# Optimization experiments

Hardware: AMD Instinct MI355X
Metric: run time of the kernel (lower is better)

The kernel has to match this reference:

```python
import jax, jax.numpy as jnp
import numpy as np

B, S, D, H, L, V, NP, GH = 2, 1024, 1024, 16, 6, 32000, 16, 64
DH = D // H
FF = int(D * 4 * 2 / 3)  # SwiGLU hidden = int(dim*ffn_expansion*2/3)


def setup_inputs() -> dict:
    key = jax.random.key(0)
    ks = jax.random.split(key, 12)
    n = lambda k, shp, s=0.02: (jax.random.normal(k, shp, jnp.float32) * s)
    # per-layer memory gate init: -3.0 .. -1.0 across layers
    gate_init = jnp.array([-3.0 + (i / (L - 1)) * 2.0 for i in range(L)], jnp.float32)
    return dict(
        input_ids=jax.random.randint(ks[0], (B, S), 0, V),
        tok_emb=n(ks[1], (V, D)),
        w_init=jnp.zeros((D,), jnp.float32),
        persistent=n(ks[2], (NP, D), 1.0),
        norm1_w=jnp.ones((L, D), jnp.float32),
        norm2_w=jnp.ones((L, D), jnp.float32),
        norm_f_w=jnp.ones((D,), jnp.float32),
        qkv_w=n(ks[3], (L, 3 * D, D)),
        q_norm_w=jnp.ones((L, DH), jnp.float32),
        k_norm_w=jnp.ones((L, DH), jnp.float32),
        gamma_w1=n(ks[4], (L, GH, D)),
        gamma_w2=n(ks[5], (L, 1, GH)),
        memory_gate=gate_init,
        w_o=n(ks[6], (L, D, D), 0.02 / 2 ** 0.5),
        ffn_w1=n(ks[7], (L, FF, D)),
        ffn_w2=n(ks[8], (L, FF, D)),
        ffn_w3=n(ks[9], (L, D, FF)),
    )


def _rms(x, w, eps=1e-6):
    return x * jax.lax.rsqrt(jnp.mean(x * x, axis=-1, keepdims=True) + eps) * w


def _rope_tables():
    inv_freq = 1.0 / (10000.0 ** (jnp.arange(0, DH, 2, dtype=jnp.float32) / DH))
    t = jnp.arange(S, dtype=jnp.float32)
    freqs = jnp.einsum('s,f->sf', t, inv_freq)  # (S, DH/2)
    return jnp.cos(freqs), jnp.sin(freqs)


def _rope(x, cos, sin):  # x: (B,H,S,DH)
    x1, x2 = jnp.split(x, 2, axis=-1)
    return jnp.concatenate([x1 * cos - x2 * sin, x2 * cos + x1 * sin], axis=-1)


def reference(input_ids, tok_emb, w_init, persistent, norm1_w, norm2_w, norm_f_w,
              qkv_w, q_norm_w, k_norm_w, gamma_w1, gamma_w2, memory_gate,
              w_o, ffn_w1, ffn_w2, ffn_w3):
    x = tok_emb[input_ids] + w_init  # (B,S,D)
    cos, sin = _rope_tables()
    causal = jnp.tril(jnp.ones((S, S), dtype=bool))  # True where k <= q
    scale = DH ** -0.5
    # persistent memory: per-head sum of key outer products M_p[h] = sum_j p_jh p_jh^T
    p = persistent.reshape(NP, H, DH)
    Mp = jnp.einsum('nhd,nhe->hde', p, p)
    for i in range(L):
        h = _rms(x, norm1_w[i])
        qkv = h @ qkv_w[i].T  # (B,S,3D)
        q, k, v = jnp.split(qkv, 3, axis=-1)
        q = q.reshape(B, S, H, DH).transpose(0, 2, 1, 3)
        k = k.reshape(B, S, H, DH).transpose(0, 2, 1, 3)
        v = v.reshape(B, S, H, DH).transpose(0, 2, 1, 3)
        q = _rms(q, q_norm_w[i])  # qk_norm
        k = _rms(k, k_norm_w[i])
        q = _rope(q, cos, sin)
        k = _rope(k, cos, sin)
        # gamma gate: Linear -> SiLU -> Linear -> Sigmoid, (B,S,1)
        g = jax.nn.sigmoid(jnp.einsum('oh,bsh->bso', gamma_w2[i],
                                      jax.nn.silu(jnp.einsum('hd,bsd->bsh', gamma_w1[i], h))))
        gk = g[..., 0]  # (B,S)
        # Omega-rule memory: q'_t = (M_p q_t + sum_{i<=t} gamma_i (k_i . q_t) k_i) / (NP + sum_{i<=t} gamma_i)
        mem_scores = jnp.einsum('bhqd,bhkd->bhqk', q, k) * gk[:, None, None, :]
        mem_scores = jnp.where(causal, mem_scores, 0.0)
        mem = jnp.einsum('bhqk,bhkd->bhqd', mem_scores, k)
        mpq = jnp.einsum('hde,bhse->bhsd', Mp, q)
        norm = NP + jnp.cumsum(gk, axis=1)  # (B,S)
        q_proj = (mpq + mem) / norm[:, None, :, None]
        gate = jax.nn.sigmoid(memory_gate[i])
        q = (1 - gate) * q + gate * q_proj
        # causal softmax attention
        attn = jnp.einsum('bhqd,bhkd->bhqk', q, k) * scale
        attn = jnp.where(causal, attn, jnp.finfo(attn.dtype).min)
        pw = jax.nn.softmax(attn, axis=-1)
        o = jnp.einsum('bhqk,bhkd->bhqd', pw, v).transpose(0, 2, 1, 3).reshape(B, S, D)
        x = x + o @ w_o[i].T
        # SwiGLU FFN
        h2 = _rms(x, norm2_w[i])
        x = x + (jax.nn.silu(h2 @ ffn_w1[i].T) * (h2 @ ffn_w2[i].T)) @ ffn_w3[i].T
    x = _rms(x, norm_f_w)
    return x @ tok_emb.T  # tied lm_head, (B,S,V)
```

## Files before the change

kernel.cpp:

```cpp
#include <hip/hip_runtime.h>
#include <hip/hip_bf16.h>
#include <math.h>

#define B 2
#define S 1024
#define D 1024
#define H 16
#define DH 64
#define NL 6
#define GH 64
#define NP 16
#define V 32000
#define FF 2730
#define FFP 2752
#define M (B*S)

typedef float fv4 __attribute__((ext_vector_type(4)));
typedef short bf16x8 __attribute__((ext_vector_type(8)));
typedef unsigned short us4 __attribute__((ext_vector_type(4)));
typedef unsigned short us;

#define MFMA16 __builtin_amdgcn_mfma_f32_16x16x32_bf16
#define G2L16(g, l) __builtin_amdgcn_global_load_lds( \
    (const __attribute__((address_space(1))) void*)(g), \
    (__attribute__((address_space(3))) void*)(l), 16, 0, 0)

__device__ __forceinline__ us f2bf(float f) {
  union { float f; unsigned u; } v; v.f = f;
  unsigned r = v.u + 0x7FFFu + ((v.u >> 16) & 1u);
  return (us)(r >> 16);
}
__device__ __forceinline__ float bf2f(us h) {
  union { unsigned u; float f; } v; v.u = ((unsigned)h) << 16;
  return v.f;
}

__device__ __forceinline__ int xcd_remap(int flat, int nwg) {
  int q = nwg >> 3, r = nwg & 7;
  int xcd = flat & 7, idx = flat >> 3;
  return (xcd < r) ? (xcd * (q + 1) + idx) : (r * (q + 1) + (xcd - r) * q + idx);
}

__global__ __launch_bounds__(256) void k_embed(const int* __restrict__ ids,
                                               const float* __restrict__ emb,
                                               const float* __restrict__ winit,
                                               float* __restrict__ x) {
  int m = blockIdx.x, t = threadIdx.x;
  int id = ids[m];
  fv4 a = *(const fv4*)(emb + (size_t)id * D + 4*t);
  fv4 w = *(const fv4*)(winit + 4*t);
  *(fv4*)(x + (size_t)m * D + 4*t) = a + w;
}

__global__ void k_rope_tables(float* __restrict__ cosT, float* __restrict__ sinT) {
  int idx = blockIdx.x * blockDim.x + threadIdx.x;
  if (idx >= S * 32) return;
  int s = idx >> 5, f = idx & 31;
  float inv = powf(10000.0f, -2.0f * (float)f / (float)DH);
  float ang = (float)s * inv;
  cosT[idx] = cosf(ang);
  sinT[idx] = sinf(ang);
}

__global__ __launch_bounds__(256) void k_mp(const float* __restrict__ pers,
                                            us* __restrict__ Mp) {
  int h = blockIdx.x, t = threadIdx.x;
  __shared__ float p[NP][DH];
  for (int i = t; i < NP * DH; i += 256) {
    int n = i / DH, dh = i % DH;
    p[n][dh] = pers[(size_t)n * D + h * DH + dh];
  }
  __syncthreads();
  for (int i = t; i < DH * DH; i += 256) {
    int d = i / DH, e = i % DH;
    float s = 0.f;
#pragma unroll
    for (int n = 0; n < NP; n++) s += p[n][d] * p[n][e];
    Mp[(size_t)h * DH * DH + i] = f2bf(s);
  }
}

__global__ __launch_bounds__(256) void k_rms(const float* __restrict__ in,
                                             const float* __restrict__ w,
                                             us* __restrict__ outb) {
  int m = blockIdx.x, t = threadIdx.x;
  fv4 v = *(const fv4*)(in + (size_t)m * D + 4*t);
  float ss = v[0]*v[0] + v[1]*v[1] + v[2]*v[2] + v[3]*v[3];
#pragma unroll
  for (int off = 32; off > 0; off >>= 1) ss += __shfl_down(ss, off);
  __shared__ float buf[4];
  if ((t & 63) == 0) buf[t >> 6] = ss;
  __syncthreads();
  float tot = buf[0] + buf[1] + buf[2] + buf[3];
  float r = rsqrtf(tot * (1.0f / (float)D) + 1e-6f);
  fv4 wv = *(const fv4*)(w + 4*t);
  fv4 res = v * r * wv;
  us4 o; o[0]=f2bf(res[0]); o[1]=f2bf(res[1]); o[2]=f2bf(res[2]); o[3]=f2bf(res[3]);
  *(us4*)(outb + (size_t)m * D + 4*t) = o;
}

__global__ __launch_bounds__(256) void k_rmsg(const float* __restrict__ in,
                                              const float* __restrict__ w,
                                              const float* __restrict__ w1,
                                              const float* __restrict__ w2,
                                              us* __restrict__ outb,
                                              float* __restrict__ gko) {
  int m = blockIdx.x, t = threadIdx.x;
  __shared__ float hrow[D];
  __shared__ float buf[4];
  __shared__ float part[4][64];
  fv4 v = *(const fv4*)(in + (size_t)m * D + 4*t);
  float ss = v[0]*v[0] + v[1]*v[1] + v[2]*v[2] + v[3]*v[3];
#pragma unroll
  for (int off = 32; off > 0; off >>= 1) ss += __shfl_down(ss, off);
  if ((t & 63) == 0) buf[t >> 6] = ss;
  __syncthreads();
  float tot = buf[0] + buf[1] + buf[2] + buf[3];
  float r = rsqrtf(tot * (1.0f / (float)D) + 1e-6f);
  fv4 wv = *(const fv4*)(w + 4*t);
  fv4 res = v * r * wv;
  us4 o; o[0]=f2bf(res[0]); o[1]=f2bf(res[1]); o[2]=f2bf(res[2]); o[3]=f2bf(res[3]);
  *(us4*)(outb + (size_t)m * D + 4*t) = o;
  *(fv4*)&hrow[4*t] = res;
  __syncthreads();
  int oo = t & 63, seg = t >> 6;
  const float* wr = w1 + (size_t)oo * D + seg * 256;
  const float* hr = hrow + seg * 256;
  float acc = 0.f;
  for (int j = 0; j < 256; j += 4) {
    fv4 wv4 = *(const fv4*)(wr + j);
    acc += wv4[0]*hr[j] + wv4[1]*hr[j+1] + wv4[2]*hr[j+2] + wv4[3]*hr[j+3];
  }
  part[seg][oo] = acc;
  __syncthreads();
  if (t < 64) {
    float dot = part[0][t] + part[1][t] + part[2][t] + part[3][t];
    float sv = dot / (1.f + expf(-dot));
    float val = sv * w2[t];
#pragma unroll
    for (int off = 32; off > 0; off >>= 1) val += __shfl_down(val, off);
    if (t == 0) gko[m] = 1.f / (1.f + expf(-val));
  }
}

__global__ __launch_bounds__(256) void k_cvt(const float* __restrict__ src,
                                             us* __restrict__ dst, int n) {
  for (size_t i = ((size_t)blockIdx.x * 256 + threadIdx.x) * 4; i < (size_t)n;
       i += (size_t)gridDim.x * 1024) {
    fv4 v = *(const fv4*)(src + i);
    us4 o; o[0]=f2bf(v[0]); o[1]=f2bf(v[1]); o[2]=f2bf(v[2]); o[3]=f2bf(v[3]);
    *(us4*)(dst + i) = o;
  }
}

#define CVT_N1 786432
#define CVT_N2 262144
#define CVT_N3 698880
#define CVT_N4 698880
#define CVT_N5 704512
__global__ __launch_bounds__(256) void k_cvtw(const float* __restrict__ s1,
                                              const float* __restrict__ s2,
                                              const float* __restrict__ s3,
                                              const float* __restrict__ s4,
                                              const float* __restrict__ s5,
                                              us* __restrict__ d1, us* __restrict__ d2,
                                              us* __restrict__ d3, us* __restrict__ d4,
                                              us* __restrict__ d5) {
  const int TOT = CVT_N1 + CVT_N2 + CVT_N3 + CVT_N4 + CVT_N5;
  for (int i = blockIdx.x * 256 + threadIdx.x; i < TOT; i += gridDim.x * 256) {
    const float* s; us* d; int j = i;
    if (j < CVT_N1) { s = s1; d = d1; }
    else if ((j -= CVT_N1) < CVT_N2) { s = s2; d = d2; }
    else if ((j -= CVT_N2) < CVT_N3) { s = s3; d = d3; }
    else if ((j -= CVT_N3) < CVT_N4) { s = s4; d = d4; }
    else {
      j -= CVT_N4;
      int r = j / (FFP/4), c = (j % (FFP/4)) * 4;
      us4 o;
#pragma unroll
      for (int q = 0; q < 4; q++) {
        int cc = c + q;
        o[q] = (cc < FF) ? f2bf(s5[(size_t)r * FF + cc]) : (us)0;
      }
      *(us4*)&d5[(size_t)r * FFP + c] = o;
      continue;
    }
    fv4 v = *(const fv4*)(s + (size_t)4 * j);
    us4 o; o[0]=f2bf(v[0]); o[1]=f2bf(v[1]); o[2]=f2bf(v[2]); o[3]=f2bf(v[3]);
    *(us4*)&d[(size_t)4 * j] = o;
  }
}

template<int EPI, int BM, int BN>
__global__ __launch_bounds__(256) void k_bgemm(const us* __restrict__ A,
                                               const us* __restrict__ W,
                                               float* __restrict__ C,
                                               int Nn, int Kk) {
  constexpr int FM = BM / 32;
  constexpr int FN = BN / 32;
  constexpr int ACW = BM / 32;
  constexpr int BCW = BN / 32;
  __shared__ __attribute__((aligned(16))) us As[BM * 64];
  __shared__ __attribute__((aligned(16))) us Bs[BN * 64];
  int t = threadIdx.x, lane = t & 63, w = t >> 6;
  int l16 = lane & 15, lkb = lane >> 4;
  int lr = lane >> 3, lc = (lane & 7) * 8;
  int gx = gridDim.x, nwg = gx * gridDim.y;
  int nf = xcd_remap(blockIdx.y * gx + blockIdx.x, nwg);
  int m0 = (nf % gx) * BM, n0 = (nf / gx) * BN;
  int wr = w >> 1, wc = w & 1;

  const us* aB[ACW]; us* aL[ACW];
  const us* bB[BCW]; us* bL[BCW];
#pragma unroll
  for (int i = 0; i < ACW; i++) {
    int chunk = w * ACW + i;
    aB[i] = A + (size_t)(m0 + chunk * 8 + lr) * Kk + lc;
    aL[i] = &As[chunk * 512];
  }
#pragma unroll
  for (int i = 0; i < BCW; i++) {
    int chunk = w * BCW + i;
    int wrow = n0 + chunk * 8 + lr;
    if (wrow >= Nn) wrow = Nn - 1;
    bB[i] = W + (size_t)wrow * Kk + lc;
    bL[i] = &Bs[chunk * 512];
  }

  fv4 acc[FM][FN] = {};
  for (int k0 = 0; k0 < Kk; k0 += 64) {
#pragma unroll
    for (int i = 0; i < ACW; i++) G2L16(aB[i] + k0, aL[i]);
#pragma unroll
    for (int i = 0; i < BCW; i++) G2L16(bB[i] + k0, bL[i]);
    __syncthreads();
#pragma unroll
    for (int kk = 0; kk < 2; kk++) {
      bf16x8 af[FM], bfh[FN];
#pragma unroll
      for (int i = 0; i < FM; i++)
        af[i] = *(const bf16x8*)&As[(wr*(BM/2) + i*16 + l16)*64 + kk*32 + lkb*8];
#pragma unroll
      for (int j = 0; j < FN; j++)
        bfh[j] = *(const bf16x8*)&Bs[(wc*(BN/2) + j*16 + l16)*64 + kk*32 + lkb*8];
#pragma unroll
      for (int i = 0; i < FM; i++)
#pragma unroll
        for (int j = 0; j < FN; j++)
          acc[i][j] = MFMA16(af[i], bfh[j], acc[i][j], 0, 0, 0);
    }
    __syncthreads();
  }

#pragma unroll
  for (int i = 0; i < FM; i++) {
    int gr0 = m0 + wr*(BM/2) + i*16 + lkb*4;
#pragma unroll
    for (int j = 0; j < FN; j++) {
      int gc = n0 + wc*(BN/2) + j*16 + l16;
      if (gc < Nn) {
#pragma unroll
        for (int r = 0; r < 4; r++) {
          size_t idx = (size_t)(gr0 + r) * Nn + gc;
          float val = acc[i][j][r];
          if (EPI == 0) C[idx] = val;
          else if (EPI == 1) C[idx] = val / (1.f + expf(-val));
          else if (EPI == 2) C[idx] += val;
          else C[idx] *= val;
        }
      }
    }
  }
}

__global__ __launch_bounds__(256) void k_qkvgemm(const us* __restrict__ A,
                                                 const us* __restrict__ W,
                                                 const float* __restrict__ qnw,
                                                 const float* __restrict__ knw,
                                                 const float* __restrict__ cosT,
                                                 const float* __restrict__ sinT,
                                                 us* __restrict__ qb,
                                                 us* __restrict__ kb,
                                                 us* __restrict__ vb) {
  const int Kk = D, Nn = 3 * D;
  __shared__ __attribute__((aligned(16))) us As[128 * 64];
  __shared__ __attribute__((aligned(16))) us Bs[128 * 64];
  int t = threadIdx.x, lane = t & 63, w = t >> 6;
  int l16 = lane & 15, lkb = lane >> 4;
  int lr = lane >> 3, lc = (lane & 7) * 8;
  int gx = gridDim.x, nwg = gx * gridDim.y;
  int nf = xcd_remap(blockIdx.y * gx + blockIdx.x, nwg);
  int m0 = (nf % gx) * 128, n0 = (nf / gx) * 128;
  int wr = w >> 1, wc = w & 1;

  const us* aB[4]; us* aL[4];
  const us* bB[4]; us* bL[4];
#pragma unroll
  for (int i = 0; i < 4; i++) {
    int chunk = w * 4 + i;
    aB[i] = A + (size_t)(m0 + chunk * 8 + lr) * Kk + lc;
    aL[i] = &As[chunk * 512];
    bB[i] = W + (size_t)(n0 + chunk * 8 + lr) * Kk + lc;
    bL[i] = &Bs[chunk * 512];
  }

  fv4 acc[4][4] = {};
  for (int k0 = 0; k0 < Kk; k0 += 64) {
#pragma unroll
    for (int i = 0; i < 4; i++) { G2L16(aB[i] + k0, aL[i]); G2L16(bB[i] + k0, bL[i]); }
    __syncthreads();
#pragma unroll
    for (int kk = 0; kk < 2; kk++) {
      bf16x8 af[4], bfh[4];
#pragma unroll
      for (int i = 0; i < 4; i++)
        af[i] = *(const bf16x8*)&As[(wr*64 + i*16 + l16)*64 + kk*32 + lkb*8];
#pragma unroll
      for (int j = 0; j < 4; j++)
        bfh[j] = *(const bf16x8*)&Bs[(wc*64 + j*16 + l16)*64 + kk*32 + lkb*8];
#pragma unroll
      for (int i = 0; i < 4; i++)
#pragma unroll
        for (int j = 0; j < 4; j++)
          acc[i][j] = MFMA16(af[i], bfh[j], acc[i][j], 0, 0, 0);
    }
    __syncthreads();
  }

  int part = n0 >> 10;
  int hd = ((n0 & 1023) + wc * 64) >> 6;
  us* dst = (part == 0) ? qb : ((part == 1) ? kb : vb);
  if (part == 2) {
#pragma unroll
    for (int i = 0; i < 4; i++)
#pragma unroll
      for (int r = 0; r < 4; r++) {
        int m = m0 + wr*64 + i*16 + lkb*4 + r;
        int b = m >> 10, s = m & 1023;
        us* drow = dst + (((size_t)(b*H + hd)) * S + s) * 64;
#pragma unroll
        for (int j = 0; j < 4; j++) drow[j*16 + l16] = f2bf(acc[i][j][r]);
      }
  } else {
    const float* nw = (part == 0) ? qnw : knw;
    float w0 = nw[l16], w1 = nw[16 + l16], w2 = nw[32 + l16], w3 = nw[48 + l16];
#pragma unroll
    for (int i = 0; i < 4; i++)
#pragma unroll
      for (int r = 0; r < 4; r++) {
        int m = m0 + wr*64 + i*16 + lkb*4 + r;
        int b = m >> 10, s = m & 1023;
        float a0 = acc[i][0][r], a1 = acc[i][1][r], a2 = acc[i][2][r], a3 = acc[i][3][r];
        float s2 = a0*a0 + a1*a1 + a2*a2 + a3*a3;
        s2 += __shfl_xor(s2, 1); s2 += __shfl_xor(s2, 2);
        s2 += __shfl_xor(s2, 4); s2 += __shfl_xor(s2, 8);
        float rs = rsqrtf(s2 * (1.0f / (float)DH) + 1e-6f);
        float v0 = a0 * rs * w0, v1 = a1 * rs * w1, v2 = a2 * rs * w2, v3 = a3 * rs * w3;
        float c0 = cosT[s*32 + l16],      sn0 = sinT[s*32 + l16];
        float c1 = cosT[s*32 + 16 + l16], sn1 = sinT[s*32 + 16 + l16];
        us* drow = dst + (((size_t)(b*H + hd)) * S + s) * 64;
        drow[l16]      = f2bf(v0 * c0 - v2 * sn0);
        drow[16 + l16] = f2bf(v1 * c1 - v3 * sn1);
        drow[32 + l16] = f2bf(v2 * c0 + v0 * sn0);
        drow[48 + l16] = f2bf(v3 * c1 + v1 * sn1);
      }
  }
}

struct G8 { const us* A; const us* W; int K; int m0; int n0; };

__device__ __forceinline__ void g8_issue(const G8& g, us* lds8, int q, int t) {
  int tile = q >> 2, h = q & 3;
  us* buf = lds8 + (size_t)(tile & 1) * 32768;
  const us* Gp = (h < 2) ? g.A : g.W;
  int rbase = ((h < 2) ? g.m0 : g.n0) + (h & 1) * 128;
  us* part = buf + (h >> 1) * 16384 + (h & 1) * 8192;
  int r8 = t >> 3;
  int sl = (((t & 7) ^ (r8 & 7)) * 8);
#pragma unroll
  for (int c = 0; c < 2; c++) {
    const us* src = Gp + (size_t)(rbase + c * 64 + r8) * g.K + tile * 64 + sl;
    us* dst = part + c * 4096 + t * 8;
    G2L16(src, dst);
  }
}

__global__ __launch_bounds__(512, 2) void k_gemm8(const us* __restrict__ A,
                                                  const us* __restrict__ W,
                                                  float* __restrict__ C,
                                                  int Nn, int Kk) {
  __shared__ __attribute__((aligned(16))) us lds8[65536];
  int t = threadIdx.x, lane = t & 63, w = t >> 6;
  int wm = w >> 2, wn = w & 3;
  int l16 = lane & 15, lkb = lane >> 4;
  int gx = gridDim.x, nwg = gx * gridDim.y;
  int nf = xcd_remap(blockIdx.y * gx + blockIdx.x, nwg);
  int m0 = (nf % gx) * 256, n0 = (nf / gx) * 256;
  G8 g{A, W, Kk, m0, n0};
  int NK = Kk >> 6, QMAX = NK * 4;

  int q = 0;
  for (; q < 7 && q < QMAX; ++q) g8_issue(g, lds8, q, t);

  fv4 acc[8][4] = {};
  int arow = wm * 128 + l16;
  int brow = wn * 64 + l16;
  int sw = l16 & 7;

  for (int T = 0; T < NK; ++T) {
    if (q < QMAX) { g8_issue(g, lds8, q, t); q++; }
    if (T == NK - 1) asm volatile("s_waitcnt vmcnt(0)" ::: "memory");
    else             asm volatile("s_waitcnt vmcnt(8)" ::: "memory");
    __builtin_amdgcn_s_barrier();
    const us* buf = lds8 + (size_t)(T & 1) * 32768;
    bf16x8 a0[8], a1[8], b0[4], b1[4];
#pragma unroll
    for (int i = 0; i < 8; i++) {
      a0[i] = *(const bf16x8*)&buf[(arow + i*16)*64 + ((lkb     ) ^ sw)*8];
      a1[i] = *(const bf16x8*)&buf[(arow + i*16)*64 + ((lkb +  4) ^ sw)*8];
    }
#pragma unroll
    for (int j = 0; j < 4; j++) {
      b0[j] = *(const bf16x8*)&buf[16384 + (brow + j*16)*64 + ((lkb    ) ^ sw)*8];
      b1[j] = *(const bf16x8*)&buf[16384 + (brow + j*16)*64 + ((lkb + 4) ^ sw)*8];
    }
    __builtin_amdgcn_s_barrier();
    __builtin_amdgcn_s_setprio(1);
#pragma unroll
    for (int i = 0; i < 8; i++)
#pragma unroll
      for (int j = 0; j < 4; j++)
        acc[i][j] = MFMA16(a0[i], b0[j], acc[i][j], 0, 0, 0);
    __builtin_amdgcn_s_setprio(0);
    if (q < QMAX) { g8_issue(g, lds8, q, t); q++; }
    if (q < QMAX) { g8_issue(g, lds8, q, t); q++; }
    if (q < QMAX) { g8_issue(g, lds8, q, t); q++; }
    __builtin_amdgcn_s_setprio(1);
#pragma unroll
    for (int i = 0; i < 8; i++)
#pragma unroll
      for (int j = 0; j < 4; j++)
        acc[i][j] = MFMA16(a1[i], b1[j], acc[i][j], 0, 0, 0);
    __builtin_amdgcn_s_setprio(0);
  }

#pragma unroll
  for (int i = 0; i < 8; i++) {
    int gr0 = m0 + wm*128 + i*16 + lkb*4;
#pragma unroll
    for (int j = 0; j < 4; j++) {
      int gc = n0 + wn*64 + j*16 + l16;
#pragma unroll
      for (int r = 0; r < 4; r++)
        C[(size_t)(gr0 + r) * Nn + gc] = acc[i][j][r];
    }
  }
}

__global__ __launch_bounds__(256) void k_ffn12(const us* __restrict__ A,
                                               const us* __restrict__ W1,
                                               const us* __restrict__ W2,
                                               us* __restrict__ Cb,
                                               int Nn, int Kk) {
  __shared__ __attribute__((aligned(16))) us As[128 * 64];
  __shared__ __attribute__((aligned(16))) us B1s[64 * 64];
  __shared__ __attribute__((aligned(16))) us B2s[64 * 64];
  int t = threadIdx.x, lane = t & 63, w = t >> 6;
  int l16 = lane & 15, lkb = lane >> 4;
  int lr = lane >> 3, lc = (lane & 7) * 8;
  int gx = gridDim.x, nwg = gx * gridDim.y;
  int nf = xcd_remap(blockIdx.y * gx + blockIdx.x, nwg);
  int m0 = (nf % gx) * 128, n0 = (nf / gx) * 64;
  int wr = w >> 1, wc = w & 1;

  const us* aB[4]; us* aL[4];
  const us* b1B[2]; us* b1L[2];
  const us* b2B[2]; us* b2L[2];
#pragma unroll
  for (int i = 0; i < 4; i++) {
    int chunk = w * 4 + i;
    aB[i] = A + (size_t)(m0 + chunk * 8 + lr) * Kk + lc;
    aL[i] = &As[chunk * 512];
  }
#pragma unroll
  for (int i = 0; i < 2; i++) {
    int chunk = w * 2 + i;
    int wrow = n0 + chunk * 8 + lr;
    if (wrow >= Nn) wrow = Nn - 1;
    b1B[i] = W1 + (size_t)wrow * Kk + lc;
    b1L[i] = &B1s[chunk * 512];
    b2B[i] = W2 + (size_t)wrow * Kk + lc;
    b2L[i] = &B2s[chunk * 512];
  }

  fv4 acc1[4][2] = {}, acc2[4][2] = {};
  for (int k0 = 0; k0 < Kk; k0 += 64) {
#pragma unroll
    for (int i = 0; i < 4; i++) G2L16(aB[i] + k0, aL[i]);
#pragma unroll
    for (int i = 0; i < 2; i++) {
      G2L16(b1B[i] + k0, b1L[i]);
      G2L16(b2B[i] + k0, b2L[i]);
    }
    __syncthreads();
#pragma unroll
    for (int kk = 0; kk < 2; kk++) {
      bf16x8 af[4], b1f[2], b2f[2];
#pragma unroll
      for (int i = 0; i < 4; i++)
        af[i] = *(const bf16x8*)&As[(wr*64 + i*16 + l16)*64 + kk*32 + lkb*8];
#pragma unroll
      for (int j = 0; j < 2; j++) {
        b1f[j] = *(const bf16x8*)&B1s[(wc*32 + j*16 + l16)*64 + kk*32 + lkb*8];
        b2f[j] = *(const bf16x8*)&B2s[(wc*32 + j*16 + l16)*64 + kk*32 + lkb*8];
      }
#pragma unroll
      for (int i = 0; i < 4; i++)
#pragma unroll
        for (int j = 0; j < 2; j++) {
          acc1[i][j] = MFMA16(af[i], b1f[j], acc1[i][j], 0, 0, 0);
          acc2[i][j] = MFMA16(af[i], b2f[j], acc2[i][j], 0, 0, 0);
        }
    }
    __syncthreads();
  }

#pragma unroll
  for (int i = 0; i < 4; i++) {
    int gr0 = m0 + wr*64 + i*16 + lkb*4;
#pragma unroll
    for (int j = 0; j < 2; j++) {
      int gc = n0 + wc*32 + j*16 + l16;
      if (gc < Nn) {
#pragma unroll
        for (int r = 0; r < 4; r++) {
          float v1 = acc1[i][j][r], v2 = acc2[i][j][r];
          float sv = v1 / (1.f + expf(-v1));
          Cb[(size_t)(gr0 + r) * FFP + gc] = f2bf(sv * v2);
        }
      }
    }
  }
}

__global__ __launch_bounds__(256) void k_tr2(const us* __restrict__ ksrc,
                                             const us* __restrict__ vsrc,
                                             us* __restrict__ kdst,
                                             us* __restrict__ vdst) {
  __shared__ __attribute__((aligned(16))) us tile[64*72];
  int st = blockIdx.x, bh = blockIdx.y, t = threadIdx.x;
  const us* src = blockIdx.z ? vsrc : ksrc;
  us* dst = blockIdx.z ? vdst : kdst;
  const us* sp = src + ((size_t)bh * S + st*64) * 64;
#pragma unroll
  for (int p = 0; p < 2; p++) {
    int idx = t + p*256;
    int r = idx >> 3, c = (idx & 7)*8;
    *(bf16x8*)&tile[r*72 + c] = *(const bf16x8*)&sp[(size_t)idx*8];
  }
  __syncthreads();
  int d = t >> 2;
#pragma unroll
  for (int cc = 0; cc < 16; cc += 8) {
    int s0 = (t & 3)*16 + cc;
    bf16x8 vv;
#pragma unroll
    for (int j2 = 0; j2 < 8; j2++) vv[j2] = (short)tile[(s0+j2)*72 + d];
    *(bf16x8*)&dst[((size_t)bh*64 + d)*S + st*64 + s0] = vv;
  }
}

__global__ __launch_bounds__(1024) void k_cumsum(const float* __restrict__ gk,
                                                 float* __restrict__ nrm) {
  int b = blockIdx.x, t = threadIdx.x;
  int lane = t & 63, wv = t >> 6;
  float s = gk[b*S + t];
#pragma unroll
  for (int off = 1; off < 64; off <<= 1) {
    float y = __shfl_up(s, off, 64);
    if (lane >= off) s += y;
  }
  __shared__ float wsum[16];
  if (lane == 63) wsum[wv] = s;
  __syncthreads();
  if (t < 16) {
    float v = wsum[t];
    float sv = v;
#pragma unroll
    for (int off = 1; off < 16; off <<= 1) {
      float y = __shfl_up(sv, off, 16);
      if (t >= off) sv += y;
    }
    wsum[t] = sv - v;
  }
  __syncthreads();
  nrm[b*S + t] = (float)NP + s + wsum[wv];
}

#define SM_OFF 24.0f
__global__ __launch_bounds__(256) void k_matt(const us* __restrict__ qb,
                                              const us* __restrict__ kb,
                                              const us* __restrict__ kbT,
                                              const us* __restrict__ vbT,
                                              const us* __restrict__ MpB,
                                              const float* __restrict__ gk,
                                              const float* __restrict__ nrm,
                                              const float* __restrict__ mg, int layer,
                                              us* __restrict__ ob) {
  int nf = xcd_remap(blockIdx.y * 8 + blockIdx.x, 256);
  int xx = nf & 7, bh = nf >> 3;
  int b = bh >> 4, hh = bh & 15;
  int t = threadIdx.x, lane = t & 63, w = t >> 6;
  int l16 = lane & 15, lg = lane >> 4;

  __shared__ __attribute__((aligned(16))) us Qs[64*72];
  __shared__ __attribute__((aligned(16))) us Ks[64*72];
  __shared__ __attribute__((aligned(16))) us Ts[64*72];
  __shared__ __attribute__((aligned(16))) us Ps[64*72];
  __shared__ float gks_[64], nrms[64];

  float gate = 1.f / (1.f + expf(-mg[layer]));

  for (int sel = 0; sel < 2; sel++) {
    int qt = sel ? (15 - xx) : xx;
    __syncthreads();

    {
      const us* src = qb + ((size_t)bh * S + qt*64) * 64;
      const us* mp = MpB + (size_t)hh * 4096;
#pragma unroll
      for (int p = 0; p < 2; p++) {
        int idx = t + p*256;
        int r = idx >> 3, c = (idx & 7) * 8;
        *(bf16x8*)&Qs[r*72 + c] = *(const bf16x8*)&src[(size_t)idx*8];
        *(bf16x8*)&Ts[r*72 + c] = *(const bf16x8*)&mp[(size_t)idx*8];
      }
      if (t < 64) nrms[t] = nrm[b*S + qt*64 + t];
    }
    __syncthreads();

    bf16x8 aq0 = *(const bf16x8*)&Qs[(16*w + l16)*72 + lg*8];
    bf16x8 aq1 = *(const bf16x8*)&Qs[(16*w + l16)*72 + 32 + lg*8];

    fv4 am[4];
#pragma unroll
    for (int j = 0; j < 4; j++) {
      bf16x8 b0 = *(const bf16x8*)&Ts[(16*j + l16)*72 + lg*8];
      bf16x8 b1 = *(const bf16x8*)&Ts[(16*j + l16)*72 + 32 + lg*8];
      fv4 z = {};
      z = MFMA16(aq0, b0, z, 0, 0, 0);
      z = MFMA16(aq1, b1, z, 0, 0, 0);
      am[j] = z;
    }

    for (int kt = 0; kt <= qt; kt++) {
      __syncthreads();
      {
        const us* ksrc = kb + ((size_t)bh * S + kt*64) * 64;
#pragma unroll
        for (int p = 0; p < 2; p++) {
          int idx = t + p*256;
          int r = idx >> 3, c = (idx & 7) * 8;
          *(bf16x8*)&Ks[r*72 + c] = *(const bf16x8*)&ksrc[(size_t)idx*8];
        }
        int d = t >> 2, c0 = (t & 3) * 16;
        const us* tsrc = kbT + ((size_t)bh*64 + d) * S + kt*64 + c0;
        *(bf16x8*)&Ts[d*72 + c0]     = *(const bf16x8*)&tsrc[0];
        *(bf16x8*)&Ts[d*72 + c0 + 8] = *(const bf16x8*)&tsrc[8];
        if (t < 64) gks_[t] = gk[b*S + kt*64 + t];
      }
      __syncthreads();
      fv4 sc[4];
#pragma unroll
      for (int j = 0; j < 4; j++) {
        bf16x8 b0 = *(const bf16x8*)&Ks[(16*j + l16)*72 + lg*8];
        bf16x8 b1 = *(const bf16x8*)&Ks[(16*j + l16)*72 + 32 + lg*8];
        fv4 z = {};
        z = MFMA16(aq0, b0, z, 0, 0, 0);
        z = MFMA16(aq1, b1, z, 0, 0, 0);
        sc[j] = z;
      }
      if (kt < qt) {
#pragma unroll
        for (int j = 0; j < 4; j++) {
          float g = gks_[16*j + l16];
#pragma unroll
          for (int r = 0; r < 4; r++)
            Ps[(16*w + lg*4 + r)*72 + 16*j + l16] = f2bf(sc[j][r] * g);
        }
      } else {
#pragma unroll
        for (int j = 0; j < 4; j++) {
          int kj = 16*j + l16;
          float g = gks_[kj];
#pragma unroll
          for (int r = 0; r < 4; r++) {
            int qi = 16*w + lg*4 + r;
            Ps[qi*72 + kj] = (kj > qi) ? (us)0 : f2bf(sc[j][r] * g);
          }
        }
      }
      bf16x8 ap0 = *(const bf16x8*)&Ps[(16*w + l16)*72 + lg*8];
      bf16x8 ap1 = *(const bf16x8*)&Ps[(16*w + l16)*72 + 32 + lg*8];
#pragma unroll
      for (int j = 0; j < 4; j++) {
        bf16x8 b0 = *(const bf16x8*)&Ts[(16*j + l16)*72 + lg*8];
        bf16x8 b1 = *(const bf16x8*)&Ts[(16*j + l16)*72 + 32 + lg*8];
        am[j] = MFMA16(ap0, b0, am[j], 0, 0, 0);
        am[j] = MFMA16(ap1, b1, am[j], 0, 0, 0);
      }
    }

#pragma unroll
    for (int j = 0; j < 4; j++)
#pragma unroll
      for (int r = 0; r < 4; r++) {
        int qi = 16*w + lg*4 + r, dj = 16*j + l16;
        float qold = bf2f(Qs[qi*72 + dj]);
        float qn = (1.f - gate) * qold + gate * (am[j][r] / nrms[qi]);
        Qs[qi*72 + dj] = f2bf(qn);
      }
    aq0 = *(const bf16x8*)&Qs[(16*w + l16)*72 + lg*8];
    aq1 = *(const bf16x8*)&Qs[(16*w + l16)*72 + 32 + lg*8];

    float lsum[4] = {};
    fv4 ao[4] = {};
    for (int kt = 0; kt <= qt; kt++) {
      __syncthreads();
      {
        const us* ksrc = kb + ((size_t)bh * S + kt*64) * 64;
#pragma unroll
        for (int p = 0; p < 2; p++) {
          int idx = t + p*256;
          int r = idx >> 3, c = (idx & 7) * 8;
          *(bf16x8*)&Ks[r*72 + c] = *(const bf16x8*)&ksrc[(size_t)idx*8];
        }
        int d = t >> 2, c0 = (t & 3) * 16;
        const us* tsrc = vbT + ((size_t)bh*64 + d) * S + kt*64 + c0;
        *(bf16x8*)&Ts[d*72 + c0]     = *(const bf16x8*)&tsrc[0];
        *(bf16x8*)&Ts[d*72 + c0 + 8] = *(const bf16x8*)&tsrc[8];
      }
      __syncthreads();
      fv4 sc[4];
#pragma unroll
      for (int j = 0; j < 4; j++) {
        bf16x8 b0 = *(const bf16x8*)&Ks[(16*j + l16)*72 + lg*8];
        bf16x8 b1 = *(const bf16x8*)&Ks[(16*j + l16)*72 + 32 + lg*8];
        fv4 z = {};
        z = MFMA16(aq0, b0, z, 0, 0, 0);
        z = MFMA16(aq1, b1, z, 0, 0, 0);
        sc[j] = z;
      }
      if (kt < qt) {
#pragma unroll
        for (int j = 0; j < 4; j++)
#pragma unroll
          for (int r = 0; r < 4; r++) {
            float p = __expf(fmaf(sc[j][r], 0.125f, -SM_OFF));
            lsum[r] += p;
            Ps[(16*w + lg*4 + r)*72 + 16*j + l16] = f2bf(p);
          }
      } else {
#pragma unroll
        for (int j = 0; j < 4; j++) {
          int kj = 16*j + l16;
#pragma unroll
          for (int r = 0; r < 4; r++) {
            int qi = 16*w + lg*4 + r;
            float p = (kj > qi) ? 0.f : __expf(fmaf(sc[j][r], 0.125f, -SM_OFF));
            lsum[r] += p;
            Ps[qi*72 + kj] = f2bf(p);
          }
        }
      }
      bf16x8 ap0 = *(const bf16x8*)&Ps[(16*w + l16)*72 + lg*8];
      bf16x8 ap1 = *(const bf16x8*)&Ps[(16*w + l16)*72 + 32 + lg*8];
#pragma unroll
      for (int j = 0; j < 4; j++) {
        bf16x8 b0 = *(const bf16x8*)&Ts[(16*j + l16)*72 + lg*8];
        bf16x8 b1 = *(const bf16x8*)&Ts[(16*j + l16)*72 + 32 + lg*8];
        ao[j] = MFMA16(ap0, b0, ao[j], 0, 0, 0);
        ao[j] = MFMA16(ap1, b1, ao[j], 0, 0, 0);
      }
    }

#pragma unroll
    for (int r = 0; r < 4; r++) {
      float l = lsum[r];
      l += __shfl_xor(l, 1);
      l += __shfl_xor(l, 2);
      l += __shfl_xor(l, 4);
      l += __shfl_xor(l, 8);
      lsum[r] = l;
    }
#pragma unroll
    for (int j = 0; j < 4; j++)
#pragma unroll
      for (int r = 0; r < 4; r++) {
        int qi = 16*w + lg*4 + r;
        ob[((size_t)b*S + qt*64 + qi) * D + hh*64 + 16*j + l16] = f2bf(ao[j][r] / lsum[r]);
      }
  }
}

extern "C" void kernel_launch(void* const* d_in, const int* in_sizes, int n_in,
                              void* d_out, int out_size, void* d_ws, size_t ws_size,
                              hipStream_t stream) {
  const int*   ids      = (const int*)d_in[0];
  const float* tok_emb  = (const float*)d_in[1];
  const float* w_init   = (const float*)d_in[2];
  const float* persist  = (const float*)d_in[3];
  const float* norm1_w  = (const float*)d_in[4];
  const float* norm2_w  = (const float*)d_in[5];
  const float* norm_f_w = (const float*)d_in[6];
  const float* qkv_w    = (const float*)d_in[7];
  const float* q_norm_w = (const float*)d_in[8];
  const float* k_norm_w = (const float*)d_in[9];
  const float* gamma_w1 = (const float*)d_in[10];
  const float* gamma_w2 = (const float*)d_in[11];
  const float* mem_gate = (const float*)d_in[12];
  const float* w_o      = (const float*)d_in[13];
  const float* ffn_w1   = (const float*)d_in[14];
  const float* ffn_w2   = (const float*)d_in[15];
  const float* ffn_w3   = (const float*)d_in[16];
  float* out = (float*)d_out;

  float* ws   = (float*)d_ws;
  float* x    = ws;
  us*    hbf  = (us*)(x + 2097152);
  float* gk   = x + 2097152 + 1048576;
  float* nrm  = gk + 2048;
  float* cosT = nrm + 2048;
  float* sinT = cosT + 32768;
  us*    MpBH = (us*)(sinT + 32768);
  float* h    = sinT + 32768 + 65536;
  float* qkv  = h + 2097152;
  us*    obf  = (us*)(qkv + 6291456);
  us*    qb   = obf + 2097152;
  us*    kb   = qb + 2097152;
  us*    vb   = kb + 2097152;
  us*    kbT  = vb + 2097152;
  us*    vbT  = kbT + 2097152;
  us*    f1bf = vbT + 2097152;
  us*    wq   = f1bf + (size_t)M*FFP;
  us*    wo   = wq + 3145728;
  us*    w1c  = wo + 1048576;
  us*    w2c  = w1c + 2795520;
  us*    w3c  = w2c + 2795520;
  us*    temb = (us*)h;

  k_embed<<<M, 256, 0, stream>>>(ids, tok_emb, w_init, x);
  k_rope_tables<<<(S*32 + 255)/256, 256, 0, stream>>>(cosT, sinT);
  k_mp<<<H, 256, 0, stream>>>(persist, MpBH);

  for (int l = 0; l < NL; l++) {
    k_cvtw<<<2048, 256, 0, stream>>>(qkv_w + (size_t)l*3*D*D, w_o + (size_t)l*D*D,
                                     ffn_w1 + (size_t)l*FF*D, ffn_w2 + (size_t)l*FF*D,
                                     ffn_w3 + (size_t)l*D*FF,
                                     wq, wo, w1c, w2c, w3c);
    k_rmsg<<<M, 256, 0, stream>>>(x, norm1_w + (size_t)l * D,
                                  gamma_w1 + (size_t)l*GH*D, gamma_w2 + (size_t)l*GH,
                                  hbf, gk);
    k_qkvgemm<<<dim3(16, 24), 256, 0, stream>>>(hbf, wq,
                                                q_norm_w + (size_t)l*DH, k_norm_w + (size_t)l*DH,
                                                cosT, sinT, qb, kb, vb);
    k_tr2<<<dim3(S/64, B*H, 2), 256, 0, stream>>>(kb, vb, kbT, vbT);
    k_cumsum<<<B, S, 0, stream>>>(gk, nrm);
    k_matt<<<dim3(8, B*H), 256, 0, stream>>>(qb, kb, kbT, vbT, MpBH, gk, nrm, mem_gate, l, obf);
    k_bgemm<2,64,64><<<dim3(M/64, D/64), 256, 0, stream>>>(obf, wo, x, D, D);
    k_rms<<<M, 256, 0, stream>>>(x, norm2_w + (size_t)l * D, hbf);
    k_ffn12<<<dim3(M/128, (FF+63)/64), 256, 0, stream>>>(hbf, w1c, w2c, f1bf, FF, D);
    k_bgemm<2,64,64><<<dim3(M/64, D/64), 256, 0, stream>>>(f1bf, w3c, x, D, FFP);
  }

  k_rms<<<M, 256, 0, stream>>>(x, norm_f_w, hbf);
  k_cvt<<<2048, 256, 0, stream>>>(tok_emb, temb, V*D);
  k_gemm8<<<dim3(8, V/256), 512, 0, stream>>>(hbf, temb, out, V, D);
}
```

Baseline: 1.738 ms.

## Double-buffer LDS with async prefetch and XOR swizzle in layer GEMMs

```diff
diff --git a/kernel.cpp b/kernel.cpp
--- a/kernel.cpp
+++ b/kernel.cpp
@@ -33,6 +33,13 @@
 __device__ __forceinline__ float bf2f(us h) {
   union { unsigned u; float f; } v; v.u = ((unsigned)h) << 16;
   return v.f;
+}
+
+template<int N> __device__ __forceinline__ void waitcnt_vm() {
+  if constexpr (N == 0)      asm volatile("s_waitcnt vmcnt(0)" ::: "memory");
+  else if constexpr (N == 4) asm volatile("s_waitcnt vmcnt(4)" ::: "memory");
+  else if constexpr (N == 8) asm volatile("s_waitcnt vmcnt(8)" ::: "memory");
+  else if constexpr (N == 6) asm volatile("s_waitcnt vmcnt(6)" ::: "memory");
 }
 
 __device__ __forceinline__ int xcd_remap(int flat, int nwg) {
@@ -191,65 +198,76 @@
   }
 }
 
+template<int ACW, int BCW>
+__device__ __forceinline__ void pg_stage(const us* __restrict__ A,
+                                         const us* __restrict__ W,
+                                         us* bufA, us* bufB,
+                                         int m0, int n0, int Nn, int Kk,
+                                         int tile, int w, int lane, int lr, int sx) {
+#pragma unroll
+  for (int i = 0; i < ACW; i++) {
+    int chunk = w * ACW + i;
+    G2L16(A + (size_t)(m0 + chunk*8 + lr) * Kk + tile*64 + sx, bufA + chunk*512 + lane*8);
+  }
+#pragma unroll
+  for (int i = 0; i < BCW; i++) {
+    int chunk = w * BCW + i;
+    int wrow = n0 + chunk*8 + lr;
+    if (wrow >= Nn) wrow = Nn - 1;
+    G2L16(W + (size_t)wrow * Kk + tile*64 + sx, bufB + chunk*512 + lane*8);
+  }
+}
+
 template<int EPI, int BM, int BN>
-__global__ __launch_bounds__(256) void k_bgemm(const us* __restrict__ A,
+__global__ __launch_bounds__(256) void k_pgemm(const us* __restrict__ A,
                                                const us* __restrict__ W,
                                                float* __restrict__ C,
                                                int Nn, int Kk) {
-  constexpr int FM = BM / 32;
-  constexpr int FN = BN / 32;
-  constexpr int ACW = BM / 32;
-  constexpr int BCW = BN / 32;
-  __shared__ __attribute__((aligned(16))) us As[BM * 64];
-  __shared__ __attribute__((aligned(16))) us Bs[BN * 64];
+  constexpr int FM = BM / 32, FN = BN / 32;
+  constexpr int ACW = BM / 32, BCW = BN / 32;
+  constexpr int L = ACW + BCW;
+  __shared__ __attribute__((aligned(16))) us lds[2][(BM + BN) * 64];
   int t = threadIdx.x, lane = t & 63, w = t >> 6;
-  int l16 = lane & 15, lkb = lane >> 4;
-  int lr = lane >> 3, lc = (lane & 7) * 8;
+  int l16 = lane & 15, lkb = lane >> 4, lr = lane >> 3;
+  int sx = ((lane & 7) ^ lr) * 8;
+  int sw = l16 & 7;
   int gx = gridDim.x, nwg = gx * gridDim.y;
   int nf = xcd_remap(blockIdx.y * gx + blockIdx.x, nwg);
   int m0 = (nf % gx) * BM, n0 = (nf / gx) * BN;
   int wr = w >> 1, wc = w & 1;
-
-  const us* aB[ACW]; us* aL[ACW];
-  const us* bB[BCW]; us* bL[BCW];
-#pragma unroll
-  for (int i = 0; i < ACW; i++) {
-    int chunk = w * ACW + i;
-    aB[i] = A + (size_t)(m0 + chunk * 8 + lr) * Kk + lc;
-    aL[i] = &As[chunk * 512];
-  }
-#pragma unroll
-  for (int i = 0; i < BCW; i++) {
-    int chunk = w * BCW + i;
-    int wrow = n0 + chunk * 8 + lr;
-    if (wrow >= Nn) wrow = Nn - 1;
-    bB[i] = W + (size_t)wrow * Kk + lc;
-    bL[i] = &Bs[chunk * 512];
-  }
+  int NK = Kk >> 6;
+
+  pg_stage<ACW,BCW>(A, W, lds[0], lds[0] + BM*64, m0, n0, Nn, Kk, 0, w, lane, lr, sx);
+  pg_stage<ACW,BCW>(A, W, lds[1], lds[1] + BM*64, m0, n0, Nn, Kk, 1, w, lane, lr, sx);
 
   fv4 acc[FM][FN] = {};
-  for (int k0 = 0; k0 < Kk; k0 += 64) {
-#pragma unroll
-    for (int i = 0; i < ACW; i++) G2L16(aB[i] + k0, aL[i]);
-#pragma unroll
-    for (int i = 0; i < BCW; i++) G2L16(bB[i] + k0, bL[i]);
-    __syncthreads();
+  for (int T = 0; T < NK; T++) {
+    if (T == NK - 1) waitcnt_vm<0>(); else waitcnt_vm<L>();
+    __builtin_amdgcn_s_barrier();
+    const us* bufA = lds[T & 1];
+    const us* bufB = bufA + BM*64;
+    bf16x8 af[2][FM], bfh[2][FN];
 #pragma unroll
     for (int kk = 0; kk < 2; kk++) {
-      bf16x8 af[FM], bfh[FN];
 #pragma unroll
       for (int i = 0; i < FM; i++)
-        af[i] = *(const bf16x8*)&As[(wr*(BM/2) + i*16 + l16)*64 + kk*32 + lkb*8];
+        af[kk][i] = *(const bf16x8*)&bufA[(wr*(BM/2) + i*16 + l16)*64 + (((kk*4+lkb)) ^ sw)*8];
 #pragma unroll
       for (int j = 0; j < FN; j++)
-        bfh[j] = *(const bf16x8*)&Bs[(wc*(BN/2) + j*16 + l16)*64 + kk*32 + lkb*8];
+        bfh[kk][j] = *(const bf16x8*)&bufB[(wc*(BN/2) + j*16 + l16)*64 + (((kk*4+lkb)) ^ sw)*8];
+    }
+    __builtin_amdgcn_s_barrier();
+    if (T + 2 < NK)
+      pg_stage<ACW,BCW>(A, W, lds[T & 1], lds[T & 1] + BM*64, m0, n0, Nn, Kk, T + 2, w, lane, lr, sx);
+    __builtin_amdgcn_s_setprio(1);
+#pragma unroll
+    for (int kk = 0; kk < 2; kk++)
 #pragma unroll
       for (int i = 0; i < FM; i++)
 #pragma unroll
         for (int j = 0; j < FN; j++)
-          acc[i][j] = MFMA16(af[i], bfh[j], acc[i][j], 0, 0, 0);
-    }
-    __syncthreads();
+          acc[i][j] = MFMA16(af[kk][i], bfh[kk][j], acc[i][j], 0, 0, 0);
+    __builtin_amdgcn_s_setprio(0);
   }
 
 #pragma unroll
@@ -264,67 +282,154 @@
           size_t idx = (size_t)(gr0 + r) * Nn + gc;
           float val = acc[i][j][r];
           if (EPI == 0) C[idx] = val;
-          else if (EPI == 1) C[idx] = val / (1.f + expf(-val));
-          else if (EPI == 2) C[idx] += val;
-          else C[idx] *= val;
+          else C[idx] += val;
         }
       }
     }
   }
 }
 
-__global__ __launch_bounds__(256) void k_qkvgemm(const us* __restrict__ A,
-                                                 const us* __restrict__ W,
-                                                 const float* __restrict__ qnw,
-                                                 const float* __restrict__ knw,
-                                                 const float* __restrict__ cosT,
-                                                 const float* __restrict__ sinT,
-                                                 us* __restrict__ qb,
-                                                 us* __restrict__ kb,
-                                                 us* __restrict__ vb) {
+__device__ __forceinline__ void pf_stage(const us* __restrict__ A,
+                                         const us* __restrict__ W1,
+                                         const us* __restrict__ W2,
+                                         us* buf, int m0, int n0, int Nn, int Kk,
+                                         int tile, int w, int lane, int lr, int sx) {
+#pragma unroll
+  for (int i = 0; i < 4; i++) {
+    int chunk = w * 4 + i;
+    G2L16(A + (size_t)(m0 + chunk*8 + lr) * Kk + tile*64 + sx, buf + chunk*512 + lane*8);
+  }
+#pragma unroll
+  for (int i = 0; i < 2; i++) {
+    int chunk = w * 2 + i;
+    int wrow = n0 + chunk*8 + lr;
+    if (wrow >= Nn) wrow = Nn - 1;
+    G2L16(W1 + (size_t)wrow * Kk + tile*64 + sx, buf + 8192 + chunk*512 + lane*8);
+    G2L16(W2 + (size_t)wrow * Kk + tile*64 + sx, buf + 12288 + chunk*512 + lane*8);
+  }
+}
+
+__global__ __launch_bounds__(256) void k_pffn12(const us* __restrict__ A,
+                                                const us* __restrict__ W1,
+                                                const us* __restrict__ W2,
+                                                us* __restrict__ Cb,
+                                                int Nn, int Kk) {
+  __shared__ __attribute__((aligned(16))) us lds[2][16384];
+  int t = threadIdx.x, lane = t & 63, w = t >> 6;
+  int l16 = lane & 15, lkb = lane >> 4, lr = lane >> 3;
+  int sx = ((lane & 7) ^ lr) * 8;
+  int sw = l16 & 7;
+  int gx = gridDim.x, nwg = gx * gridDim.y;
+  int nf = xcd_remap(blockIdx.y * gx + blockIdx.x, nwg);
+  int m0 = (nf % gx) * 128, n0 = (nf / gx) * 64;
+  int wr = w >> 1, wc = w & 1;
+  int NK = Kk >> 6;
+
+  pf_stage(A, W1, W2, lds[0], m0, n0, Nn, Kk, 0, w, lane, lr, sx);
+  pf_stage(A, W1, W2, lds[1], m0, n0, Nn, Kk, 1, w, lane, lr, sx);
+
+  fv4 acc1[4][2] = {}, acc2[4][2] = {};
+  for (int T = 0; T < NK; T++) {
+    if (T == NK - 1) waitcnt_vm<0>(); else waitcnt_vm<8>();
+    __builtin_amdgcn_s_barrier();
+    const us* buf = lds[T & 1];
+    bf16x8 af[2][4], b1f[2][2], b2f[2][2];
+#pragma unroll
+    for (int kk = 0; kk < 2; kk++) {
+#pragma unroll
+      for (int i = 0; i < 4; i++)
+        af[kk][i] = *(const bf16x8*)&buf[(wr*64 + i*16 + l16)*64 + ((kk*4+lkb) ^ sw)*8];
+#pragma unroll
+      for (int j = 0; j < 2; j++) {
+        b1f[kk][j] = *(const bf16x8*)&buf[8192  + (wc*32 + j*16 + l16)*64 + ((kk*4+lkb) ^ sw)*8];
+        b2f[kk][j] = *(const bf16x8*)&buf[12288 + (wc*32 + j*16 + l16)*64 + ((kk*4+lkb) ^ sw)*8];
+      }
+    }
+    __builtin_amdgcn_s_barrier();
+    if (T + 2 < NK)
+      pf_stage(A, W1, W2, lds[T & 1], m0, n0, Nn, Kk, T + 2, w, lane, lr, sx);
+    __builtin_amdgcn_s_setprio(1);
+#pragma unroll
+    for (int kk = 0; kk < 2; kk++)
+#pragma unroll
+      for (int i = 0; i < 4; i++)
+#pragma unroll
+        for (int j = 0; j < 2; j++) {
+          acc1[i][j] = MFMA16(af[kk][i], b1f[kk][j], acc1[i][j], 0, 0, 0);
+          acc2[i][j] = MFMA16(af[kk][i], b2f[kk][j], acc2[i][j], 0, 0, 0);
+        }
+    __builtin_amdgcn_s_setprio(0);
+  }
+
+#pragma unroll
+  for (int i = 0; i < 4; i++) {
+    int gr0 = m0 + wr*64 + i*16 + lkb*4;
+#pragma unroll
+    for (int j = 0; j < 2; j++) {
+      int gc = n0 + wc*32 + j*16 + l16;
+      if (gc < Nn) {
+#pragma unroll
+        for (int r = 0; r < 4; r++) {
+          float v1 = acc1[i][j][r], v2 = acc2[i][j][r];
+          float sv = v1 / (1.f + expf(-v1));
+          Cb[(size_t)(gr0 + r) * FFP + gc] = f2bf(sv * v2);
+        }
+      }
+    }
+  }
+}
+
+__global__ __launch_bounds__(256) void k_pqkv(const us* __restrict__ A,
+                                              const us* __restrict__ W,
+                                              const float* __restrict__ qnw,
+                                              const float* __restrict__ knw,
+                                              const float* __restrict__ cosT,
+                                              const float* __restrict__ sinT,
+                                              us* __restrict__ qb,
+                                              us* __restrict__ kb,
+                                              us* __restrict__ vb) {
   const int Kk = D, Nn = 3 * D;
-  __shared__ __attribute__((aligned(16))) us As[128 * 64];
-  __shared__ __attribute__((aligned(16))) us Bs[128 * 64];
+  __shared__ __attribute__((aligned(16))) us lds[2][16384];
   int t = threadIdx.x, lane = t & 63, w = t >> 6;
-  int l16 = lane & 15, lkb = lane >> 4;
-  int lr = lane >> 3, lc = (lane & 7) * 8;
+  int l16 = lane & 15, lkb = lane >> 4, lr = lane >> 3;
+  int sx = ((lane & 7) ^ lr) * 8;
+  int sw = l16 & 7;
   int gx = gridDim.x, nwg = gx * gridDim.y;
   int nf = xcd_remap(blockIdx.y * gx + blockIdx.x, nwg);
   int m0 = (nf % gx) * 128, n0 = (nf / gx) * 128;
   int wr = w >> 1, wc = w & 1;
-
-  const us* aB[4]; us* aL[4];
-  const us* bB[4]; us* bL[4];
-#pragma unroll
-  for (int i = 0; i < 4; i++) {
-    int chunk = w * 4 + i;
-    aB[i] = A + (size_t)(m0 + chunk * 8 + lr) * Kk + lc;
-    aL[i] = &As[chunk * 512];
-    bB[i] = W + (size_t)(n0 + chunk * 8 + lr) * Kk + lc;
-    bL[i] = &Bs[chunk * 512];
-  }
+  int NK = Kk >> 6;
+
+  pg_stage<4,4>(A, W, lds[0], lds[0] + 8192, m0, n0, Nn, Kk, 0, w, lane, lr, sx);
+  pg_stage<4,4>(A, W, lds[1], lds[1] + 8192, m0, n0, Nn, Kk, 1, w, lane, lr, sx);
 
   fv4 acc[4][4] = {};
-  for (int k0 = 0; k0 < Kk; k0 += 64) {
-#pragma unroll
-    for (int i = 0; i < 4; i++) { G2L16(aB[i] + k0, aL[i]); G2L16(bB[i] + k0, bL[i]); }
-    __syncthreads();
+  for (int T = 0; T < NK; T++) {
+    if (T == NK - 1) waitcnt_vm<0>(); else waitcnt_vm<8>();
+    __builtin_amdgcn_s_barrier();
+    const us* bufA = lds[T & 1];
+    const us* bufB = bufA + 8192;
+    bf16x8 af[2][4], bfh[2][4];
 #pragma unroll
     for (int kk = 0; kk < 2; kk++) {
-      bf16x8 af[4], bfh[4];
+#pragma unroll
+      for (int i = 0; i < 4; i++) {
+        af[kk][i]  = *(const bf16x8*)&bufA[(wr*64 + i*16 + l16)*64 + ((kk*4+lkb) ^ sw)*8];
+        bfh[kk][i] = *(const bf16x8*)&bufB[(wc*64 + i*16 + l16)*64 + ((kk*4+lkb) ^ sw)*8];
+      }
+    }
+    __builtin_amdgcn_s_barrier();
+    if (T + 2 < NK)
+      pg_stage<4,4>(A, W, lds[T & 1], lds[T & 1] + 8192, m0, n0, Nn, Kk, T + 2, w, lane, lr, sx);
+    __builtin_amdgcn_s_setprio(1);
+#pragma unroll
+    for (int kk = 0; kk < 2; kk++)
 #pragma unroll
       for (int i = 0; i < 4; i++)
-        af[i] = *(const bf16x8*)&As[(wr*64 + i*16 + l16)*64 + kk*32 + lkb*8];
-#pragma unroll
-      for (int j = 0; j < 4; j++)
-        bfh[j] = *(const bf16x8*)&Bs[(wc*64 + j*16 + l16)*64 + kk*32 + lkb*8];
-#pragma unroll
-      for (int i = 0; i < 4; i++)
 #pragma unroll
         for (int j = 0; j < 4; j++)
-          acc[i][j] = MFMA16(af[i], bfh[j], acc[i][j], 0, 0, 0);
-    }
-    __syncthreads();
+          acc[i][j] = MFMA16(af[kk][i], bfh[kk][j], acc[i][j], 0, 0, 0);
+    __builtin_amdgcn_s_setprio(0);
   }
 
   int part = n0 >> 10;
@@ -453,92 +558,6 @@
 #pragma unroll
       for (int r = 0; r < 4; r++)
         C[(size_t)(gr0 + r) * Nn + gc] = acc[i][j][r];
-    }
-  }
-}
-
-__global__ __launch_bounds__(256) void k_ffn12(const us* __restrict__ A,
-                                               const us* __restrict__ W1,
-                                               const us* __restrict__ W2,
-                                               us* __restrict__ Cb,
-                                               int Nn, int Kk) {
-  __shared__ __attribute__((aligned(16))) us As[128 * 64];
-  __shared__ __attribute__((aligned(16))) us B1s[64 * 64];
-  __shared__ __attribute__((aligned(16))) us B2s[64 * 64];
-  int t = threadIdx.x, lane = t & 63, w = t >> 6;
-  int l16 = lane & 15, lkb = lane >> 4;
-  int lr = lane >> 3, lc = (lane & 7) * 8;
-  int gx = gridDim.x, nwg = gx * gridDim.y;
-  int nf = xcd_remap(blockIdx.y * gx + blockIdx.x, nwg);
-  int m0 = (nf % gx) * 128, n0 = (nf / gx) * 64;
-  int wr = w >> 1, wc = w & 1;
-
-  const us* aB[4]; us* aL[4];
-  const us* b1B[2]; us* b1L[2];
-  const us* b2B[2]; us* b2L[2];
-#pragma unroll
-  for (int i = 0; i < 4; i++) {
-    int chunk = w * 4 + i;
-    aB[i] = A + (size_t)(m0 + chunk * 8 + lr) * Kk + lc;
-    aL[i] = &As[chunk * 512];
-  }
-#pragma unroll
-  for (int i = 0; i < 2; i++) {
-    int chunk = w * 2 + i;
-    int wrow = n0 + chunk * 8 + lr;
-    if (wrow >= Nn) wrow = Nn - 1;
-    b1B[i] = W1 + (size_t)wrow * Kk + lc;
-    b1L[i] = &B1s[chunk * 512];
-    b2B[i] = W2 + (size_t)wrow * Kk + lc;
-    b2L[i] = &B2s[chunk * 512];
-  }
-
-  fv4 acc1[4][2] = {}, acc2[4][2] = {};
-  for (int k0 = 0; k0 < Kk; k0 += 64) {
-#pragma unroll
-    for (int i = 0; i < 4; i++) G2L16(aB[i] + k0, aL[i]);
-#pragma unroll
-    for (int i = 0; i < 2; i++) {
-      G2L16(b1B[i] + k0, b1L[i]);
-      G2L16(b2B[i] + k0, b2L[i]);
-    }
-    __syncthreads();
-#pragma unroll
-    for (int kk = 0; kk < 2; kk++) {
-      bf16x8 af[4], b1f[2], b2f[2];
-#pragma unroll
-      for (int i = 0; i < 4; i++)
-        af[i] = *(const bf16x8*)&As[(wr*64 + i*16 + l16)*64 + kk*32 + lkb*8];
-#pragma unroll
-      for (int j = 0; j < 2; j++) {
-        b1f[j] = *(const bf16x8*)&B1s[(wc*32 + j*16 + l16)*64 + kk*32 + lkb*8];
-        b2f[j] = *(const bf16x8*)&B2s[(wc*32 + j*16 + l16)*64 + kk*32 + lkb*8];
-      }
-#pragma unroll
-      for (int i = 0; i < 4; i++)
-#pragma unroll
-        for (int j = 0; j < 2; j++) {
-          acc1[i][j] = MFMA16(af[i], b1f[j], acc1[i][j], 0, 0, 0);
-          acc2[i][j] = MFMA16(af[i], b2f[j], acc2[i][j], 0, 0, 0);
-        }
-    }
-    __syncthreads();
-  }
-
-#pragma unroll
-  for (int i = 0; i < 4; i++) {
-    int gr0 = m0 + wr*64 + i*16 + lkb*4;
-#pragma unroll
-    for (int j = 0; j < 2; j++) {
-      int gc = n0 + wc*32 + j*16 + l16;
-      if (gc < Nn) {
-#pragma unroll
-        for (int r = 0; r < 4; r++) {
-          float v1 = acc1[i][j][r], v2 = acc2[i][j][r];
-          float sv = v1 / (1.f + expf(-v1));
-          Cb[(size_t)(gr0 + r) * FFP + gc] = f2bf(sv * v2);
-        }
-      }
     }
   }
 }
@@ -861,16 +880,16 @@
     k_rmsg<<<M, 256, 0, stream>>>(x, norm1_w + (size_t)l * D,
                                   gamma_w1 + (size_t)l*GH*D, gamma_w2 + (size_t)l*GH,
                                   hbf, gk);
-    k_qkvgemm<<<dim3(16, 24), 256, 0, stream>>>(hbf, wq,
-                                                q_norm_w + (size_t)l*DH, k_norm_w + (size_t)l*DH,
-                                                cosT, sinT, qb, kb, vb);
+    k_pqkv<<<dim3(16, 24), 256, 0, stream>>>(hbf, wq,
+                                             q_norm_w + (size_t)l*DH, k_norm_w + (size_t)l*DH,
+                                             cosT, sinT, qb, kb, vb);
     k_tr2<<<dim3(S/64, B*H, 2), 256, 0, stream>>>(kb, vb, kbT, vbT);
     k_cumsum<<<B, S, 0, stream>>>(gk, nrm);
     k_matt<<<dim3(8, B*H), 256, 0, stream>>>(qb, kb, kbT, vbT, MpBH, gk, nrm, mem_gate, l, obf);
-    k_bgemm<2,64,64><<<dim3(M/64, D/64), 256, 0, stream>>>(obf, wo, x, D, D);
+    k_pgemm<2,64,64><<<dim3(M/64, D/64), 256, 0, stream>>>(obf, wo, x, D, D);
     k_rms<<<M, 256, 0, stream>>>(x, norm2_w + (size_t)l * D, hbf);
-    k_ffn12<<<dim3(M/128, (FF+63)/64), 256, 0, stream>>>(hbf, w1c, w2c, f1bf, FF, D);
-    k_bgemm<2,64,64><<<dim3(M/64, D/64), 256, 0, stream>>>(f1bf, w3c, x, D, FFP);
+    k_pffn12<<<dim3(M/128, (FF+63)/64), 256, 0, stream>>>(hbf, w1c, w2c, f1bf, FF, D);
+    k_pgemm<2,64,64><<<dim3(M/64, D/64), 256, 0, stream>>>(f1bf, w3c, x, D, FFP);
   }
 
   k_rms<<<M, 256, 0, stream>>>(x, norm_f_w, hbf);
```

Result: faster. 1.501 ms (-13.7%).
